# Kernel tuning notes

Hardware: AMD Instinct MI355X
Metric: run time of the kernel (lower is better)

Reference implementation:

```python
import jax, jax.numpy as jnp
import numpy as np
import math

B, S, H = 8, 1024, 1024
NH, DH = 16, 64  # MULTI_HEAD, HIDDEN_SIZE_HEAD


def setup_inputs() -> dict:
    key = jax.random.key(0)
    ks = jax.random.split(key, 12)
    scale = 0.02
    inp = {
        "v": jax.random.normal(ks[0], (B, S, H), jnp.float32),
        "k": jax.random.normal(ks[1], (B, S, H), jnp.float32),
        "q": jax.random.normal(ks[2], (B, S, H), jnp.float32),
        # True = masked position (masked_fill semantics)
        "mask": jax.random.bernoulli(ks[3], 0.1, (B, 1, 1, S)),
        "Wq": jax.random.normal(ks[4], (H, H), jnp.float32) * scale,
        "bq": jnp.zeros((H,), jnp.float32),
        "Wk": jax.random.normal(ks[5], (H, H), jnp.float32) * scale,
        "bk": jnp.zeros((H,), jnp.float32),
        "Wv": jax.random.normal(ks[6], (H, H), jnp.float32) * scale,
        "bv": jnp.zeros((H,), jnp.float32),
        "Wm": jax.random.normal(ks[7], (H, H), jnp.float32) * scale,
        "bm": jnp.zeros((H,), jnp.float32),
    }
    return inp


def _split_heads(x):
    # [B, S, H] -> [B, NH, S, DH]
    b, s, _ = x.shape
    return x.reshape(b, s, NH, DH).transpose(0, 2, 1, 3)


def reference(v, k, q, mask, Wq, bq, Wk, bk, Wv, bv, Wm, bm):
    # QKV projections (torch Linear: x @ W.T + b)
    qh = _split_heads(q @ Wq.T + bq)  # [B, NH, S, DH]
    kh = _split_heads(k @ Wk.T + bk)
    vh = _split_heads(v @ Wv.T + bv)

    scores = jnp.einsum("bhqd,bhkd->bhqk", qh, kh) / math.sqrt(DH)
    scores = jnp.where(mask, jnp.float32(-1e9), scores)
    att = jax.nn.softmax(scores, axis=-1)
    # dropout rate 0.0 (eval mode) -> identity
    ctx = jnp.einsum("bhqk,bhkd->bhqd", att, vh)  # [B, NH, S, DH]

    b = q.shape[0]
    merged = ctx.transpose(0, 2, 1, 3).reshape(b, -1, NH * DH)  # [B, S, H]
    return merged @ Wm.T + bm
```

## Files before the change

kernel.cpp:

```cpp
#include <hip/hip_runtime.h>
#include <hip/hip_bf16.h>

#define Bn 8
#define Sn 1024
#define Hn 1024
#define NHn 16
#define DHn 64
#define Mn (Bn * Sn)

typedef unsigned short u16;
typedef short bf16x8 __attribute__((ext_vector_type(8)));
typedef unsigned short u16x4 __attribute__((ext_vector_type(4)));
typedef float f32x4 __attribute__((ext_vector_type(4)));

__device__ __forceinline__ u16 f2bf(float x) {
  union { __hip_bfloat16 h; u16 u; } cv;
  cv.h = __float2bfloat16(x);
  return cv.u;
}

__device__ __forceinline__ void async_ld16(void* lds, const void* g) {
  __builtin_amdgcn_global_load_lds(
      (const __attribute__((address_space(1))) void*)g,
      (__attribute__((address_space(3))) void*)lds, 16, 0, 0);
}

__global__ __launch_bounds__(256) void sniff_k(const void* __restrict__ mask,
                                               int* __restrict__ flags) {
  __shared__ int viol;
  if (threadIdx.x == 0) viol = 0;
  __syncthreads();
  const unsigned* mw = (const unsigned*)mask;
  int vb = 0;
#pragma unroll
  for (int j = 0; j < 8; ++j) {
    unsigned v = mw[threadIdx.x * 8 + j];
    if (v > 1u) vb |= 1;
    if ((v & 0xFEFEFEFEu) != 0u) vb |= 2;
    if (!(v == 0u || v == 0x3F800000u)) vb |= 4;
    unsigned h0 = v & 0xFFFFu, h1 = v >> 16;
    if (!((h0 == 0u || h0 == 0x3F80u) && (h1 == 0u || h1 == 0x3F80u))) vb |= 8;
  }
  if (vb) atomicOr(&viol, vb);
  __syncthreads();
  if (threadIdx.x == 0) {
    int mt;
    if (!(viol & 1))      mt = 0;
    else if (!(viol & 2)) mt = 1;
    else if (!(viol & 4)) mt = 3;
    else if (!(viol & 8)) mt = 2;
    else                  mt = 0;
    flags[1] = mt;
  }
}

__global__ __launch_bounds__(256) void convert3(
    const float* __restrict__ a, const float* __restrict__ b,
    const float* __restrict__ c, u16* __restrict__ da,
    u16* __restrict__ db, u16* __restrict__ dc) {
  const int seg = blockIdx.x >> 12;
  const int bid = blockIdx.x & 4095;
  const float* s = seg == 0 ? a : seg == 1 ? b : c;
  u16* d        = seg == 0 ? da : seg == 1 ? db : dc;
  const int i = (bid * 256 + threadIdx.x) * 8;
  f32x4 lo = *(const f32x4*)(s + i);
  f32x4 hi = *(const f32x4*)(s + i + 4);
  bf16x8 o;
#pragma unroll
  for (int j = 0; j < 4; ++j) { o[j] = (short)f2bf(lo[j]); o[4 + j] = (short)f2bf(hi[j]); }
  *(bf16x8*)(d + i) = o;
}

__global__ __launch_bounds__(256) void convertW(
    const float* __restrict__ a, const float* __restrict__ b,
    const float* __restrict__ c, const float* __restrict__ e,
    u16* __restrict__ da, u16* __restrict__ db,
    u16* __restrict__ dc, u16* __restrict__ de) {
  const int seg = blockIdx.x >> 9;
  const int bid = blockIdx.x & 511;
  const float* s = seg == 0 ? a : seg == 1 ? b : seg == 2 ? c : e;
  u16* d        = seg == 0 ? da : seg == 1 ? db : seg == 2 ? dc : de;
  const int i = (bid * 256 + threadIdx.x) * 8;
  f32x4 lo = *(const f32x4*)(s + i);
  f32x4 hi = *(const f32x4*)(s + i + 4);
  bf16x8 o;
#pragma unroll
  for (int j = 0; j < 4; ++j) { o[j] = (short)f2bf(lo[j]); o[4 + j] = (short)f2bf(hi[j]); }
  *(bf16x8*)(d + i) = o;
}

template <int OMODE>
__global__ __launch_bounds__(256) void gemm_bt(
    const u16* __restrict__ X, const u16* __restrict__ W,
    const float* __restrict__ bias, void* __restrict__ O, float scale)
{
  __shared__ __attribute__((aligned(16))) u16 As[128 * 32];
  __shared__ __attribute__((aligned(16))) u16 Bs[128 * 32];
  const int tid  = threadIdx.x;
  const int wave = tid >> 6;
  const int lane = tid & 63;
  const int ln   = lane & 15;
  const int quad = lane >> 4;
  const int m0 = blockIdx.x * 128;
  const int n0 = blockIdx.y * 128;
  const int wm = (wave & 1) * 64;
  const int wn = (wave >> 1) * 64;
  const int r0 = tid >> 2;
  const int oc = (tid & 3) * 8;
  char* A0 = (char*)As + wave * 1024;
  char* A1 = (char*)As + 4096 + wave * 1024;
  char* B0 = (char*)Bs + wave * 1024;
  char* B1 = (char*)Bs + 4096 + wave * 1024;

  f32x4 acc[4][4] = {};

  for (int k0 = 0; k0 < 1024; k0 += 32) {
    async_ld16(A0, X + (size_t)(m0 + r0) * 1024 + k0 + oc);
    async_ld16(A1, X + (size_t)(m0 + 64 + r0) * 1024 + k0 + oc);
    async_ld16(B0, W + (size_t)(n0 + r0) * 1024 + k0 + oc);
    async_ld16(B1, W + (size_t)(n0 + 64 + r0) * 1024 + k0 + oc);
    __syncthreads();
    bf16x8 af[4], bf[4];
#pragma unroll
    for (int t = 0; t < 4; ++t)
      af[t] = *(const bf16x8*)&As[(wm + t * 16 + ln) * 32 + quad * 8];
#pragma unroll
    for (int t = 0; t < 4; ++t)
      bf[t] = *(const bf16x8*)&Bs[(wn + t * 16 + ln) * 32 + quad * 8];
#pragma unroll
    for (int i = 0; i < 4; ++i)
#pragma unroll
      for (int j = 0; j < 4; ++j)
        acc[i][j] = __builtin_amdgcn_mfma_f32_16x16x32_bf16(af[i], bf[j], acc[i][j], 0, 0, 0);
    __syncthreads();
  }

  if (OMODE == 2) {
    const int bb = m0 >> 10;
    const int sb = m0 & 1023;
#pragma unroll
    for (int j = 0; j < 4; ++j) {
      const int col = n0 + wn + j * 16 + ln;
      const float bv = bias[col];
#pragma unroll
      for (int i = 0; i < 4; ++i) {
        const int sl = sb + wm + i * 16 + quad * 4;
        u16x4 pk;
#pragma unroll
        for (int r = 0; r < 4; ++r) pk[r] = f2bf((acc[i][j][r] + bv) * scale);
        *(u16x4*)&((u16*)O)[((size_t)(bb * 1024 + col)) * 1024 + sl] = pk;
      }
    }
  } else {
#pragma unroll
    for (int j = 0; j < 4; ++j) {
      const int col = n0 + wn + j * 16 + ln;
      const float bv = bias[col];
#pragma unroll
      for (int i = 0; i < 4; ++i) {
        const int rowb = m0 + wm + i * 16 + quad * 4;
#pragma unroll
        for (int r = 0; r < 4; ++r) {
          const float val = (acc[i][j][r] + bv) * scale;
          const size_t idx = (size_t)(rowb + r) * 1024 + col;
          if (OMODE == 1) ((float*)O)[idx] = val;
          else            ((u16*)O)[idx]   = f2bf(val);
        }
      }
    }
  }
}

__global__ __launch_bounds__(256, 3) void attn(
    const u16* __restrict__ Qb, const u16* __restrict__ Kb,
    const u16* __restrict__ Vbt, const void* __restrict__ mask,
    const int* __restrict__ flags, u16* __restrict__ Ctx)
{
  __shared__ __attribute__((aligned(16))) u16 Ks[128 * 64];
  __shared__ __attribute__((aligned(16))) u16 Vt[64 * 128];
  __shared__ __attribute__((aligned(16))) u16 Pl[4][16 * 128];
  __shared__ __attribute__((aligned(16))) float maskf[Sn];

  const int tid  = threadIdx.x;
  const int wave = tid >> 6;
  const int lane = tid & 63;
  const int ln   = lane & 15;
  const int quad = lane >> 4;
  const int bx  = blockIdx.x;
  const int x   = bx & 7;
  const int qt  = (bx >> 3) & 15;
  const int grp = bx >> 7;
  const int bh  = grp * 8 + x;
  const int b   = bh >> 4;
  const int h   = bh & 15;

  const int mt = flags[1];
  for (int i = tid; i < Sn; i += 256) {
    const int idx = b * Sn + i;
    int nz;
    if (mt == 0)      nz = ((const int*)mask)[idx] != 0;
    else if (mt == 1) nz = ((const signed char*)mask)[idx] != 0;
    else if (mt == 2) nz = ((const u16*)mask)[idx] != 0;
    else              nz = ((const unsigned*)mask)[idx] != 0;
    maskf[i] = nz ? -1e9f : 0.0f;
  }

  const size_t qoff = (size_t)(b * Sn + qt * 64 + wave * 16 + ln) * Hn + h * DHn;
  bf16x8 qf0 = *(const bf16x8*)&Qb[qoff + quad * 8];
  bf16x8 qf1 = *(const bf16x8*)&Qb[qoff + 32 + quad * 8];

  float mrun[4], lrun[4];
#pragma unroll
  for (int r = 0; r < 4; ++r) { mrun[r] = -INFINITY; lrun[r] = 0.0f; }
  f32x4 acc[4] = {};

  const int kr = tid >> 1, kh = tid & 1;
  const int vd = tid >> 2, vs = tid & 3;
  char* pw  = (char*)Pl[wave];
  char* KsB = (char*)Ks;
  char* VtB = (char*)Vt;

  const int kwb = kr * 128 + kh * 64;
  const int ksw = (kr & 7) << 4;
  const int vwb = vd * 256 + vs * 64;
  const int vsw = (vd & 7) << 4;
  const int rsw = (ln & 7) << 4;

  for (int t8 = 0; t8 < 8; ++t8) {
    const int kv0 = t8 * 128;
    __syncthreads();
    {
      const u16* g = &Kb[(size_t)(b * Sn + kv0 + kr) * Hn + h * DHn + kh * 32];
#pragma unroll
      for (int j = 0; j < 4; ++j)
        *(bf16x8*)(KsB + ((kwb + j * 16) ^ ksw)) = *(const bf16x8*)(g + j * 8);
    }
    {
      const u16* g = &Vbt[(size_t)(b * Sn + h * DHn + vd) * Sn + kv0 + vs * 32];
#pragma unroll
      for (int j = 0; j < 4; ++j)
        *(bf16x8*)(VtB + ((vwb + j * 16) ^ vsw)) = *(const bf16x8*)(g + j * 8);
    }
    __syncthreads();

    f32x4 sc[8];
#pragma unroll
    for (int t = 0; t < 8; ++t) {
      const int rb = (t * 16 + ln) * 128;
      bf16x8 kf0 = *(const bf16x8*)(KsB + ((rb + quad * 16) ^ rsw));
      bf16x8 kf1 = *(const bf16x8*)(KsB + ((rb + 64 + quad * 16) ^ rsw));
      f32x4 z = {};
      z = __builtin_amdgcn_mfma_f32_16x16x32_bf16(qf0, kf0, z, 0, 0, 0);
      z = __builtin_amdgcn_mfma_f32_16x16x32_bf16(qf1, kf1, z, 0, 0, 0);
      sc[t] = z;
    }
    float mf[8];
#pragma unroll
    for (int t = 0; t < 8; ++t) mf[t] = maskf[kv0 + t * 16 + ln];
#pragma unroll
    for (int t = 0; t < 8; ++t)
#pragma unroll
      for (int r = 0; r < 4; ++r) sc[t][r] += mf[t];

    float al[4], mx[4];
#pragma unroll
    for (int r = 0; r < 4; ++r) {
      float v = sc[0][r];
#pragma unroll
      for (int t = 1; t < 8; ++t) v = fmaxf(v, sc[t][r]);
      v = fmaxf(v, __shfl_xor(v, 1));
      v = fmaxf(v, __shfl_xor(v, 2));
      v = fmaxf(v, __shfl_xor(v, 4));
      v = fmaxf(v, __shfl_xor(v, 8));
      const float mnew = fmaxf(mrun[r], v);
      al[r] = __expf(mrun[r] - mnew);
      mrun[r] = mnew;
      mx[r] = mnew;
    }
#pragma unroll
    for (int r = 0; r < 4; ++r) {
      float s = 0.0f;
#pragma unroll
      for (int t = 0; t < 8; ++t) {
        const float p = __expf(sc[t][r] - mx[r]);
        sc[t][r] = p;
        s += p;
      }
      s += __shfl_xor(s, 1);
      s += __shfl_xor(s, 2);
      s += __shfl_xor(s, 4);
      s += __shfl_xor(s, 8);
      lrun[r] = lrun[r] * al[r] + s;
    }
#pragma unroll
    for (int t = 0; t < 8; ++t)
#pragma unroll
      for (int r = 0; r < 4; ++r) {
        const int prow = quad * 4 + r;
        *(u16*)(pw + ((prow * 256 + (t * 16 + ln) * 2) ^ ((prow & 7) << 4))) =
            f2bf(sc[t][r]);
      }
#pragma unroll
    for (int dt = 0; dt < 4; ++dt)
#pragma unroll
      for (int r = 0; r < 4; ++r) acc[dt][r] *= al[r];
    bf16x8 pa[4];
#pragma unroll
    for (int c = 0; c < 4; ++c)
      pa[c] = *(const bf16x8*)(pw + ((ln * 256 + c * 64 + quad * 16) ^ rsw));
#pragma unroll
    for (int dt = 0; dt < 4; ++dt) {
      const int vrb = (dt * 16 + ln) * 256;
#pragma unroll
      for (int c = 0; c < 4; ++c) {
        bf16x8 vb = *(const bf16x8*)(VtB + ((vrb + c * 64 + quad * 16) ^ rsw));
        acc[dt] = __builtin_amdgcn_mfma_f32_16x16x32_bf16(pa[c], vb, acc[dt], 0, 0, 0);
      }
    }
  }

#pragma unroll
  for (int dt = 0; dt < 4; ++dt)
#pragma unroll
    for (int r = 0; r < 4; ++r) {
      const int s = qt * 64 + wave * 16 + quad * 4 + r;
      Ctx[(size_t)(b * Sn + s) * Hn + h * DHn + dt * 16 + ln] = f2bf(acc[dt][r] / lrun[r]);
    }
}

extern "C" void kernel_launch(void* const* d_in, const int* in_sizes, int n_in,
                              void* d_out, int out_size, void* d_ws, size_t ws_size,
                              hipStream_t stream) {
  const float* v    = (const float*)d_in[0];
  const float* k    = (const float*)d_in[1];
  const float* q    = (const float*)d_in[2];
  const void*  mask = d_in[3];
  const float* Wq   = (const float*)d_in[4];
  const float* bq   = (const float*)d_in[5];
  const float* Wk   = (const float*)d_in[6];
  const float* bk   = (const float*)d_in[7];
  const float* Wv   = (const float*)d_in[8];
  const float* bv   = (const float*)d_in[9];
  const float* Wm   = (const float*)d_in[10];
  const float* bm   = (const float*)d_in[11];

  char* ws = (char*)d_ws;
  u16* qc  = (u16*)(ws);
  u16* kc  = (u16*)(ws + (16u << 20));
  u16* vc  = (u16*)(ws + (32u << 20));
  u16* Wqc = (u16*)(ws + (48u << 20));
  u16* Wkc = Wqc + (1u << 20);
  u16* Wvc = Wkc + (1u << 20);
  u16* Wmc = Wvc + (1u << 20);
  int* flags = (int*)(ws + (56u << 20));
  u16* Vbt = qc;
  u16* Cx  = kc;
  u16* Qb  = (u16*)d_out;
  u16* Kb  = Qb + (size_t)Mn * Hn;

  sniff_k<<<1, 256, 0, stream>>>(mask, flags);
  convert3<<<3 * 4096, 256, 0, stream>>>(q, k, v, qc, kc, vc);
  convertW<<<4 * 512, 256, 0, stream>>>(Wq, Wk, Wv, Wm, Wqc, Wkc, Wvc, Wmc);

  dim3 grid(Mn / 128, Hn / 128), blk(256);
  gemm_bt<0><<<grid, blk, 0, stream>>>(qc, Wqc, bq, Qb, 0.125f);
  gemm_bt<0><<<grid, blk, 0, stream>>>(kc, Wkc, bk, Kb, 1.0f);
  gemm_bt<2><<<grid, blk, 0, stream>>>(vc, Wvc, bv, Vbt, 1.0f);
  attn<<<dim3(Bn * NHn * (Sn / 64)), blk, 0, stream>>>(Qb, Kb, Vbt, mask, flags, Cx);
  gemm_bt<1><<<grid, blk, 0, stream>>>(Cx, Wmc, bm, d_out, 1.0f);
}
```

Measured before the change: 378.1 us.

## Read K and V fragments directly from global memory in attention kernel

Removes the shared-memory staging of K and V tiles in the attention kernel. Each wave now loads its MFMA operands straight from global memory, relying on L1/L2 caching for reuse across the four waves. This drops two block barriers per KV tile and frees LDS, so occupancy is raised to four blocks per CU. The cost is four times the global/cache load traffic for K and V, since every wave fetches the full tile, and load latency is exposed with no explicit prefetch.

```diff
diff --git a/kernel.cpp b/kernel.cpp
--- a/kernel.cpp
+++ b/kernel.cpp
@@ -171,13 +171,11 @@
   }
 }
 
-__global__ __launch_bounds__(256, 3) void attn(
+__global__ __launch_bounds__(256, 4) void attn(
     const u16* __restrict__ Qb, const u16* __restrict__ Kb,
     const u16* __restrict__ Vbt, const void* __restrict__ mask,
     const int* __restrict__ flags, u16* __restrict__ Ctx)
 {
-  __shared__ __attribute__((aligned(16))) u16 Ks[128 * 64];
-  __shared__ __attribute__((aligned(16))) u16 Vt[64 * 128];
   __shared__ __attribute__((aligned(16))) u16 Pl[4][16 * 128];
   __shared__ __attribute__((aligned(16))) float maskf[Sn];
 
@@ -204,6 +202,7 @@
     else              nz = ((const unsigned*)mask)[idx] != 0;
     maskf[i] = nz ? -1e9f : 0.0f;
   }
+  __syncthreads();
 
   const size_t qoff = (size_t)(b * Sn + qt * 64 + wave * 16 + ln) * Hn + h * DHn;
   bf16x8 qf0 = *(const bf16x8*)&Qb[qoff + quad * 8];
@@ -214,41 +213,21 @@
   for (int r = 0; r < 4; ++r) { mrun[r] = -INFINITY; lrun[r] = 0.0f; }
   f32x4 acc[4] = {};
 
-  const int kr = tid >> 1, kh = tid & 1;
-  const int vd = tid >> 2, vs = tid & 3;
-  char* pw  = (char*)Pl[wave];
-  char* KsB = (char*)Ks;
-  char* VtB = (char*)Vt;
-
-  const int kwb = kr * 128 + kh * 64;
-  const int ksw = (kr & 7) << 4;
-  const int vwb = vd * 256 + vs * 64;
-  const int vsw = (vd & 7) << 4;
+  char* pw = (char*)Pl[wave];
   const int rsw = (ln & 7) << 4;
+
+  const u16* kbase = Kb  + (size_t)(b * Sn + ln) * Hn + h * DHn + quad * 8;
+  const u16* vbase = Vbt + (size_t)(b * Sn + h * DHn + ln) * Sn + quad * 8;
 
   for (int t8 = 0; t8 < 8; ++t8) {
     const int kv0 = t8 * 128;
-    __syncthreads();
-    {
-      const u16* g = &Kb[(size_t)(b * Sn + kv0 + kr) * Hn + h * DHn + kh * 32];
-#pragma unroll
-      for (int j = 0; j < 4; ++j)
-        *(bf16x8*)(KsB + ((kwb + j * 16) ^ ksw)) = *(const bf16x8*)(g + j * 8);
-    }
-    {
-      const u16* g = &Vbt[(size_t)(b * Sn + h * DHn + vd) * Sn + kv0 + vs * 32];
-#pragma unroll
-      for (int j = 0; j < 4; ++j)
-        *(bf16x8*)(VtB + ((vwb + j * 16) ^ vsw)) = *(const bf16x8*)(g + j * 8);
-    }
-    __syncthreads();
 
     f32x4 sc[8];
 #pragma unroll
     for (int t = 0; t < 8; ++t) {
-      const int rb = (t * 16 + ln) * 128;
-      bf16x8 kf0 = *(const bf16x8*)(KsB + ((rb + quad * 16) ^ rsw));
-      bf16x8 kf1 = *(const bf16x8*)(KsB + ((rb + 64 + quad * 16) ^ rsw));
+      const u16* kp = kbase + (size_t)(kv0 + t * 16) * Hn;
+      bf16x8 kf0 = *(const bf16x8*)(kp);
+      bf16x8 kf1 = *(const bf16x8*)(kp + 32);
       f32x4 z = {};
       z = __builtin_amdgcn_mfma_f32_16x16x32_bf16(qf0, kf0, z, 0, 0, 0);
       z = __builtin_amdgcn_mfma_f32_16x16x32_bf16(qf1, kf1, z, 0, 0, 0);
@@ -310,10 +289,10 @@
       pa[c] = *(const bf16x8*)(pw + ((ln * 256 + c * 64 + quad * 16) ^ rsw));
 #pragma unroll
     for (int dt = 0; dt < 4; ++dt) {
-      const int vrb = (dt * 16 + ln) * 256;
+      const u16* vp = vbase + (size_t)(dt * 16) * Sn + kv0;
 #pragma unroll
       for (int c = 0; c < 4; ++c) {
-        bf16x8 vb = *(const bf16x8*)(VtB + ((vrb + c * 64 + quad * 16) ^ rsw));
+        bf16x8 vb = *(const bf16x8*)(vp + c * 32);
         acc[dt] = __builtin_amdgcn_mfma_f32_16x16x32_bf16(pa[c], vb, acc[dt], 0, 0, 0);
       }
     }
```

Measured after the change: 499.5 us. +32.1%, slower.
